# Optimization experiments

Hardware: AMD Instinct MI355X
Metric: run time of the kernel (lower is better)

Reference implementation:

```python
import jax, jax.numpy as jnp
import numpy as np

D_MODEL = 256
D_HIDDEN = 1024
B, S = 4, 32768


def setup_inputs() -> dict:
    key = jax.random.key(0)
    k_x, k_m, k_w1, k_b1, k_w2, k_b2 = jax.random.split(key, 6)
    x = jax.random.normal(k_x, (B, S, D_MODEL), dtype=jnp.float32)
    # graph_dependency: binary connectivity mask [d_hidden, d_model]
    mask = jax.random.randint(k_m, (D_HIDDEN, D_MODEL), 0, 2, dtype=jnp.int32)
    lim1 = 1.0 / np.sqrt(D_MODEL)
    lim2 = 1.0 / np.sqrt(D_HIDDEN)
    w1 = jax.random.uniform(k_w1, (D_HIDDEN, D_MODEL), jnp.float32, -lim1, lim1)
    b1 = jax.random.uniform(k_b1, (D_HIDDEN,), jnp.float32, -lim1, lim1)
    # reserve=True: maps d_hidden -> d_model with transposed mask
    w2 = jax.random.uniform(k_w2, (D_MODEL, D_HIDDEN), jnp.float32, -lim2, lim2)
    b2 = jax.random.uniform(k_b2, (D_MODEL,), jnp.float32, -lim2, lim2)
    return {"x": x, "w1": w1, "b1": b1, "w2": w2, "b2": b2, "mask": mask}


def reference(x, w1, b1, w2, b2, mask):
    m = mask.astype(x.dtype)                      # [H, D]
    # fc1: graph-masked linear d_model -> d_hidden
    h = jnp.einsum('bsd,hd->bsh', x, w1 * m) + b1  # [B, S, H]
    h = jax.nn.relu(h)
    # fc2 (reserve): graph-masked linear d_hidden -> d_model, transposed mask
    y = jnp.einsum('bsh,dh->bsd', h, w2 * m.T) + b2  # [B, S, D]
    return y
```

## Files before the change

kernel.cpp:

```cpp
#include <hip/hip_runtime.h>


#define D_MODEL 256
#define D_HID   1024
#define MT      128
#define NCHUNK  32
#define CHUNK_ELEMS 8192

typedef __attribute__((ext_vector_type(8))) short short8;
typedef __attribute__((ext_vector_type(16))) float f32x16;

__device__ __forceinline__ unsigned short f2bf(float f) {
  union { float f; unsigned int u; } v; v.f = f;
  unsigned int u = v.u;
  return (unsigned short)((u + 0x7FFFu + ((u >> 16) & 1u)) >> 16);
}

__device__ __forceinline__ void async16(void* lds, const void* g) {
  __builtin_amdgcn_global_load_lds(
      (const __attribute__((address_space(1))) unsigned int*)g,
      (__attribute__((address_space(3))) unsigned int*)lds,
      16, 0, 0);
}

__global__ __launch_bounds__(256) void prep_weights(
    const float* __restrict__ w1, const float* __restrict__ w2,
    const int* __restrict__ mask,
    unsigned short* __restrict__ W1p, unsigned short* __restrict__ W2p)
{
  int t = blockIdx.x * 256 + threadIdx.x;
  if (t < 32768) {
    int c    = t >> 10;
    int kf   = (t >> 6) & 15;
    int lane = t & 63;
    int h = c * 32 + (lane & 31);
    int k = kf * 16 + (lane >> 5) * 8;
    const float* wp = w1 + h * 256 + k;
    const int*   mp = mask + h * 256 + k;
    short8 v;
    #pragma unroll
    for (int j = 0; j < 8; ++j) v[j] = (short)(mp[j] ? f2bf(wp[j]) : 0);
    *(short8*)(W1p + (size_t)t * 8) = v;
  } else {
    int s    = t - 32768;
    int c    = s >> 10;
    int cf   = (s >> 7) & 7;
    int kf2  = (s >> 6) & 1;
    int lane = s & 63;
    int n = cf * 32 + (lane & 31);
    int h = c * 32 + kf2 * 16 + (lane >> 5) * 8;
    short8 v;
    #pragma unroll
    for (int j = 0; j < 8; ++j)
      v[j] = (short)(mask[(h + j) * 256 + n] ? f2bf(w2[n * 1024 + h + j]) : 0);
    *(short8*)(W2p + (size_t)s * 8) = v;
  }
}

__global__ __launch_bounds__(256, 2) void ffd_fused(
    const float* __restrict__ X, const float* __restrict__ b1,
    const float* __restrict__ b2,
    const unsigned short* __restrict__ W1p, const unsigned short* __restrict__ W2p,
    float* __restrict__ Y)
{
  __shared__ unsigned short sW1[2][CHUNK_ELEMS];
  __shared__ unsigned short sW2[2][CHUNK_ELEMS];
  __shared__ unsigned short sHc[4][1024];

  const int tid  = threadIdx.x;
  const int lane = tid & 63;
  const int w    = tid >> 6;
  const int l32  = lane & 31;
  const int q2   = lane >> 5;

  const long rowBase = (long)blockIdx.x * MT + w * 32;

  short8 xf[16];
  const float* xrow = X + (rowBase + l32) * D_MODEL;
  #pragma unroll
  for (int kf = 0; kf < 16; ++kf) {
    const float4 f0 = *(const float4*)(xrow + kf * 16 + q2 * 8);
    const float4 f1 = *(const float4*)(xrow + kf * 16 + q2 * 8 + 4);
    short8 v;
    v[0] = (short)f2bf(f0.x); v[1] = (short)f2bf(f0.y);
    v[2] = (short)f2bf(f0.z); v[3] = (short)f2bf(f0.w);
    v[4] = (short)f2bf(f1.x); v[5] = (short)f2bf(f1.y);
    v[6] = (short)f2bf(f1.z); v[7] = (short)f2bf(f1.w);
    xf[kf] = v;
  }

  f32x16 acc[8];
  #pragma unroll
  for (int i = 0; i < 8; ++i) {
    #pragma unroll
    for (int j = 0; j < 16; ++j) acc[i][j] = 0.f;
  }

  unsigned short* sHw = sHc[w];
  const int xorw = (l32 & 14) << 2;

  {
    const unsigned short* g1 = W1p + tid * 8;
    const unsigned short* g2 = W2p + tid * 8;
    #pragma unroll
    for (int i = 0; i < 4; ++i) {
      async16(&sW1[0][i * 2048 + tid * 8], g1 + i * 2048);
      async16(&sW2[0][i * 2048 + tid * 8], g2 + i * 2048);
    }
  }
  __syncthreads();

  for (int c = 0; c < NCHUNK; ++c) {
    const int cur = c & 1;

    if (c + 1 < NCHUNK) {
      const unsigned short* g1 = W1p + (size_t)(c + 1) * CHUNK_ELEMS + tid * 8;
      const unsigned short* g2 = W2p + (size_t)(c + 1) * CHUNK_ELEMS + tid * 8;
      unsigned short* d1 = &sW1[cur ^ 1][tid * 8];
      unsigned short* d2 = &sW2[cur ^ 1][tid * 8];
      #pragma unroll
      for (int i = 0; i < 4; ++i) {
        async16(d1 + i * 2048, g1 + i * 2048);
        async16(d2 + i * 2048, g2 + i * 2048);
      }
    }
    const float bb = b1[c * 32 + l32];

    f32x16 hh;
    #pragma unroll
    for (int j = 0; j < 16; ++j) hh[j] = 0.f;
    #pragma unroll
    for (int kf = 0; kf < 16; ++kf) {
      short8 bf = *(const short8*)&sW1[cur][kf * 512 + lane * 8];
      hh = __builtin_amdgcn_mfma_f32_32x32x16_bf16(xf[kf], bf, hh, 0, 0, 0);
    }

    #pragma unroll
    for (int r = 0; r < 16; ++r) {
      int rr = (r & 3) + 8 * (r >> 2) + 4 * q2;
      float v = hh[r] + bb;
      v = v > 0.f ? v : 0.f;
      sHw[(rr * 32 + l32) ^ ((rr & 14) << 2)] = f2bf(v);
    }
    __threadfence_block();

    #pragma unroll
    for (int kf2 = 0; kf2 < 2; ++kf2) {
      short8 af = *(const short8*)&sHw[(l32 * 32 + kf2 * 16 + q2 * 8) ^ xorw];
      #pragma unroll
      for (int cf = 0; cf < 8; ++cf) {
        short8 bf2 = *(const short8*)&sW2[cur][(cf * 2 + kf2) * 512 + lane * 8];
        acc[cf] = __builtin_amdgcn_mfma_f32_32x32x16_bf16(af, bf2, acc[cf], 0, 0, 0);
      }
    }

    __syncthreads();
  }

  #pragma unroll
  for (int cf = 0; cf < 8; ++cf) {
    int col = cf * 32 + l32;
    float bias = b2[col];
    #pragma unroll
    for (int r = 0; r < 16; ++r) {
      long row = rowBase + (r & 3) + 8 * (r >> 2) + 4 * q2;
      Y[row * D_MODEL + col] = acc[cf][r] + bias;
    }
  }
}

extern "C" void kernel_launch(void* const* d_in, const int* in_sizes, int n_in,
                              void* d_out, int out_size, void* d_ws, size_t ws_size,
                              hipStream_t stream) {
  const float* x    = (const float*)d_in[0];
  const float* w1   = (const float*)d_in[1];
  const float* b1   = (const float*)d_in[2];
  const float* w2   = (const float*)d_in[3];
  const float* b2   = (const float*)d_in[4];
  const int*   mask = (const int*)d_in[5];

  unsigned short* W1p = (unsigned short*)d_ws;
  unsigned short* W2p = W1p + (size_t)D_HID * D_MODEL;
  float* Y = (float*)d_out;

  prep_weights<<<256, 256, 0, stream>>>(w1, w2, mask, W1p, W2p);
  ffd_fused<<<131072 / MT, 256, 0, stream>>>(x, b1, b2, W1p, W2p, Y);
}
```

Before: 170.7 us.

## Repartition fc2 so each wave owns output columns across all block rows

In fc2, each wave now computes 64 output columns for all 128 rows of the block, instead of all 256 columns for its own 32 rows. The hidden activations are shared through a block-wide LDS buffer, which adds an extra __syncthreads per chunk. In exchange, each wave loads only its slice of W2 into registers once per chunk rather than re-reading the full W2 chunk from LDS per wave. fc1 is also split into two independent accumulator chains to break the MFMA dependency chain, and s_setprio is raised around the MFMA sections.

```diff
diff --git a/kernel.cpp b/kernel.cpp
--- a/kernel.cpp
+++ b/kernel.cpp
@@ -65,7 +65,7 @@
 {
   __shared__ unsigned short sW1[2][CHUNK_ELEMS];
   __shared__ unsigned short sW2[2][CHUNK_ELEMS];
-  __shared__ unsigned short sHc[4][1024];
+  __shared__ unsigned short sHc[MT * 32];
 
   const int tid  = threadIdx.x;
   const int lane = tid & 63;
@@ -73,7 +73,8 @@
   const int l32  = lane & 31;
   const int q2   = lane >> 5;
 
-  const long rowBase = (long)blockIdx.x * MT + w * 32;
+  const long blockRow = (long)blockIdx.x * MT;
+  const long rowBase  = blockRow + w * 32;
 
   short8 xf[16];
   const float* xrow = X + (rowBase + l32) * D_MODEL;
@@ -89,15 +90,13 @@
     xf[kf] = v;
   }
 
-  f32x16 acc[8];
+  f32x16 acc[2][4];
   #pragma unroll
-  for (int i = 0; i < 8; ++i) {
-    #pragma unroll
-    for (int j = 0; j < 16; ++j) acc[i][j] = 0.f;
-  }
-
-  unsigned short* sHw = sHc[w];
-  const int xorw = (l32 & 14) << 2;
+  for (int i = 0; i < 2; ++i)
+    #pragma unroll
+    for (int g = 0; g < 4; ++g)
+      #pragma unroll
+      for (int j = 0; j < 16; ++j) acc[i][g][j] = 0.f;
 
   {
     const unsigned short* g1 = W1p + tid * 8;
@@ -126,45 +125,62 @@
     }
     const float bb = b1[c * 32 + l32];
 
-    f32x16 hh;
-    #pragma unroll
-    for (int j = 0; j < 16; ++j) hh[j] = 0.f;
-    #pragma unroll
-    for (int kf = 0; kf < 16; ++kf) {
-      short8 bf = *(const short8*)&sW1[cur][kf * 512 + lane * 8];
-      hh = __builtin_amdgcn_mfma_f32_32x32x16_bf16(xf[kf], bf, hh, 0, 0, 0);
-    }
+    f32x16 h0, h1;
+    #pragma unroll
+    for (int j = 0; j < 16; ++j) { h0[j] = 0.f; h1[j] = 0.f; }
+    __builtin_amdgcn_s_setprio(1);
+    #pragma unroll
+    for (int kf = 0; kf < 8; ++kf) {
+      short8 bfa = *(const short8*)&sW1[cur][kf * 512 + lane * 8];
+      short8 bfb = *(const short8*)&sW1[cur][(kf + 8) * 512 + lane * 8];
+      h0 = __builtin_amdgcn_mfma_f32_32x32x16_bf16(xf[kf],     bfa, h0, 0, 0, 0);
+      h1 = __builtin_amdgcn_mfma_f32_32x32x16_bf16(xf[kf + 8], bfb, h1, 0, 0, 0);
+    }
+    __builtin_amdgcn_s_setprio(0);
 
     #pragma unroll
     for (int r = 0; r < 16; ++r) {
-      int rr = (r & 3) + 8 * (r >> 2) + 4 * q2;
-      float v = hh[r] + bb;
+      int R = w * 32 + (r & 3) + 8 * (r >> 2) + 4 * q2;
+      float v = h0[r] + h1[r] + bb;
       v = v > 0.f ? v : 0.f;
-      sHw[(rr * 32 + l32) ^ ((rr & 14) << 2)] = f2bf(v);
-    }
-    __threadfence_block();
-
-    #pragma unroll
-    for (int kf2 = 0; kf2 < 2; ++kf2) {
-      short8 af = *(const short8*)&sHw[(l32 * 32 + kf2 * 16 + q2 * 8) ^ xorw];
-      #pragma unroll
-      for (int cf = 0; cf < 8; ++cf) {
-        short8 bf2 = *(const short8*)&sW2[cur][(cf * 2 + kf2) * 512 + lane * 8];
-        acc[cf] = __builtin_amdgcn_mfma_f32_32x32x16_bf16(af, bf2, acc[cf], 0, 0, 0);
+      sHc[(R * 32 + l32) ^ ((R & 14) << 2)] = f2bf(v);
+    }
+    __syncthreads();
+
+    short8 bf2[2][2];
+    #pragma unroll
+    for (int kf2 = 0; kf2 < 2; ++kf2)
+      #pragma unroll
+      for (int cfl = 0; cfl < 2; ++cfl)
+        bf2[kf2][cfl] = *(const short8*)&sW2[cur][((w * 2 + cfl) * 2 + kf2) * 512 + lane * 8];
+
+    __builtin_amdgcn_s_setprio(1);
+    #pragma unroll
+    for (int rg = 0; rg < 4; ++rg) {
+      #pragma unroll
+      for (int kf2 = 0; kf2 < 2; ++kf2) {
+        int R = rg * 32 + l32;
+        short8 af = *(const short8*)&sHc[(R * 32 + kf2 * 16 + q2 * 8) ^ ((R & 14) << 2)];
+        acc[0][rg] = __builtin_amdgcn_mfma_f32_32x32x16_bf16(af, bf2[kf2][0], acc[0][rg], 0, 0, 0);
+        acc[1][rg] = __builtin_amdgcn_mfma_f32_32x32x16_bf16(af, bf2[kf2][1], acc[1][rg], 0, 0, 0);
       }
     }
+    __builtin_amdgcn_s_setprio(0);
 
     __syncthreads();
   }
 
   #pragma unroll
-  for (int cf = 0; cf < 8; ++cf) {
-    int col = cf * 32 + l32;
+  for (int cfl = 0; cfl < 2; ++cfl) {
+    int col = w * 64 + cfl * 32 + l32;
     float bias = b2[col];
     #pragma unroll
-    for (int r = 0; r < 16; ++r) {
-      long row = rowBase + (r & 3) + 8 * (r >> 2) + 4 * q2;
-      Y[row * D_MODEL + col] = acc[cf][r] + bias;
+    for (int rg = 0; rg < 4; ++rg) {
+      #pragma unroll
+      for (int r = 0; r < 16; ++r) {
+        long row = blockRow + rg * 32 + (r & 3) + 8 * (r >> 2) + 4 * q2;
+        Y[row * D_MODEL + col] = acc[cfl][rg][r] + bias;
+      }
     }
   }
 }
```

After: 208.7 us. 22.3% more time.

## Keep hidden activations in registers via transposed GEMM1 and permlane swaps

Applied to the files above, without the earlier changes.

GEMM1 now swaps its operands so the hidden tile comes out transposed. The relu output is packed with v_cvt_pk_bf16 and rearranged with v_permlane32_swap into the A-operand layout for GEMM2, so the per-wave LDS round trip for hidden activations and its fence go away. GEMM1 is split into two independent accumulator chains, b1 is staged into LDS once per block, and s_setprio wraps the MFMA loops. The risks are extra registers from the two accumulators and getting the lane permutation correct.

```diff
diff --git a/kernel.cpp b/kernel.cpp
--- a/kernel.cpp
+++ b/kernel.cpp
@@ -9,11 +9,22 @@
 
 typedef __attribute__((ext_vector_type(8))) short short8;
 typedef __attribute__((ext_vector_type(16))) float f32x16;
+typedef __attribute__((ext_vector_type(4))) unsigned int uint4v;
 
 __device__ __forceinline__ unsigned short f2bf(float f) {
   union { float f; unsigned int u; } v; v.f = f;
   unsigned int u = v.u;
   return (unsigned short)((u + 0x7FFFu + ((u >> 16) & 1u)) >> 16);
+}
+
+__device__ __forceinline__ unsigned cvtpk_bf16(float lo, float hi) {
+  unsigned r;
+  asm("v_cvt_pk_bf16_f32 %0, %1, %2" : "=v"(r) : "v"(lo), "v"(hi));
+  return r;
+}
+
+__device__ __forceinline__ void plswap(unsigned &a, unsigned &b) {
+  asm("v_permlane32_swap_b32 %0, %1" : "+v"(a), "+v"(b));
 }
 
 __device__ __forceinline__ void async16(void* lds, const void* g) {
@@ -65,7 +76,7 @@
 {
   __shared__ unsigned short sW1[2][CHUNK_ELEMS];
   __shared__ unsigned short sW2[2][CHUNK_ELEMS];
-  __shared__ unsigned short sHc[4][1024];
+  __shared__ float sB1[D_HID];
 
   const int tid  = threadIdx.x;
   const int lane = tid & 63;
@@ -91,14 +102,11 @@
 
   f32x16 acc[8];
   #pragma unroll
-  for (int i = 0; i < 8; ++i) {
+  for (int i = 0; i < 8; ++i)
     #pragma unroll
     for (int j = 0; j < 16; ++j) acc[i][j] = 0.f;
-  }
-
-  unsigned short* sHw = sHc[w];
-  const int xorw = (l32 & 14) << 2;
-
+
+  async16(&sB1[tid * 4], b1 + tid * 4);
   {
     const unsigned short* g1 = W1p + tid * 8;
     const unsigned short* g2 = W2p + tid * 8;
@@ -124,35 +132,50 @@
         async16(d2 + i * 2048, g2 + i * 2048);
       }
     }
-    const float bb = b1[c * 32 + l32];
-
-    f32x16 hh;
-    #pragma unroll
-    for (int j = 0; j < 16; ++j) hh[j] = 0.f;
-    #pragma unroll
-    for (int kf = 0; kf < 16; ++kf) {
-      short8 bf = *(const short8*)&sW1[cur][kf * 512 + lane * 8];
-      hh = __builtin_amdgcn_mfma_f32_32x32x16_bf16(xf[kf], bf, hh, 0, 0, 0);
-    }
-
+
+    float4 bb[4];
+    #pragma unroll
+    for (int g = 0; g < 4; ++g)
+      bb[g] = *(const float4*)&sB1[c * 32 + 4 * q2 + 8 * g];
+
+    f32x16 h0, h1;
+    #pragma unroll
+    for (int j = 0; j < 16; ++j) { h0[j] = 0.f; h1[j] = 0.f; }
+    __builtin_amdgcn_s_setprio(1);
+    #pragma unroll
+    for (int kf = 0; kf < 8; ++kf) {
+      short8 wa = *(const short8*)&sW1[cur][kf * 512 + lane * 8];
+      short8 wb = *(const short8*)&sW1[cur][(kf + 8) * 512 + lane * 8];
+      h0 = __builtin_amdgcn_mfma_f32_32x32x16_bf16(wa, xf[kf],     h0, 0, 0, 0);
+      h1 = __builtin_amdgcn_mfma_f32_32x32x16_bf16(wb, xf[kf + 8], h1, 0, 0, 0);
+    }
+    __builtin_amdgcn_s_setprio(0);
+
+    float v[16];
     #pragma unroll
     for (int r = 0; r < 16; ++r) {
-      int rr = (r & 3) + 8 * (r >> 2) + 4 * q2;
-      float v = hh[r] + bb;
-      v = v > 0.f ? v : 0.f;
-      sHw[(rr * 32 + l32) ^ ((rr & 14) << 2)] = f2bf(v);
-    }
-    __threadfence_block();
-
-    #pragma unroll
-    for (int kf2 = 0; kf2 < 2; ++kf2) {
-      short8 af = *(const short8*)&sHw[(l32 * 32 + kf2 * 16 + q2 * 8) ^ xorw];
-      #pragma unroll
-      for (int cf = 0; cf < 8; ++cf) {
-        short8 bf2 = *(const short8*)&sW2[cur][(cf * 2 + kf2) * 512 + lane * 8];
-        acc[cf] = __builtin_amdgcn_mfma_f32_32x32x16_bf16(af, bf2, acc[cf], 0, 0, 0);
-      }
-    }
+      float t = h0[r] + h1[r] + bb[r >> 2][r & 3];
+      v[r] = t > 0.f ? t : 0.f;
+    }
+
+    unsigned W0 = cvtpk_bf16(v[0],  v[1]),  W1 = cvtpk_bf16(v[2],  v[3]);
+    unsigned W2 = cvtpk_bf16(v[4],  v[5]),  W3 = cvtpk_bf16(v[6],  v[7]);
+    unsigned W4 = cvtpk_bf16(v[8],  v[9]),  W5 = cvtpk_bf16(v[10], v[11]);
+    unsigned W6 = cvtpk_bf16(v[12], v[13]), W7 = cvtpk_bf16(v[14], v[15]);
+    plswap(W0, W2); plswap(W1, W3); plswap(W4, W6); plswap(W5, W7);
+    union { uint4v u; short8 s; } A0, A1;
+    A0.u = (uint4v){W0, W1, W2, W3};
+    A1.u = (uint4v){W4, W5, W6, W7};
+
+    __builtin_amdgcn_s_setprio(1);
+    #pragma unroll
+    for (int cf = 0; cf < 8; ++cf) {
+      short8 b0 = *(const short8*)&sW2[cur][(cf * 2 + 0) * 512 + lane * 8];
+      short8 b1f = *(const short8*)&sW2[cur][(cf * 2 + 1) * 512 + lane * 8];
+      acc[cf] = __builtin_amdgcn_mfma_f32_32x32x16_bf16(A0.s, b0,  acc[cf], 0, 0, 0);
+      acc[cf] = __builtin_amdgcn_mfma_f32_32x32x16_bf16(A1.s, b1f, acc[cf], 0, 0, 0);
+    }
+    __builtin_amdgcn_s_setprio(0);
 
     __syncthreads();
   }
```

Result: faster. 163.8 us (-4.0%).
